# Kernel optimization log

Measured on AMD Instinct MI355X. Metric: run time of the kernel, lower is better.

Reference implementation:

```python
import jax, jax.numpy as jnp
import numpy as np

# Static problem sizes (see shape_source)
B, D, H, W = 2, 16, 64, 64          # batch, sparse_shape = grid_size[::-1]
NV = 20000                           # active voxels per batch sample
CIN = 16                             # input_channels
THRESH = 0.5                         # FOCAL_THRESHOLD (used for kernel-offset mask)
EPS = 1e-3                           # BatchNorm eps from norm_fn
K_FORE = int(NV * THRESH)            # topk split: top int(N*threshold) voxels are foreground
# kernel_offsets: [[i,j,k] for i,j,k in (-1..1)^3] minus [0,0,0], applied to [z,y,x]
OFFSETS = [(i, j, k) for i in range(-1, 2) for j in range(-1, 2) for k in range(-1, 2) if (i, j, k) != (0, 0, 0)]


def _conv(x, w):
    # dense 3x3x3 conv == SubMConv3d math at active sites (inactive cells hold zeros)
    return jax.lax.conv_general_dilated(x, w, (1, 1, 1), 'SAME',
                                        dimension_numbers=('NDHWC', 'DHWIO', 'NDHWC'))


def _bn(x, g, b, m, v):
    # eval-mode BatchNorm1d over voxel features
    return (x - m) * (g * jax.lax.rsqrt(v + EPS)) + b


def setup_inputs() -> dict:
    rng = np.random.default_rng(0)
    coords = []
    for b in range(B):  # unique voxel coords per sample (spconv requires unique indices)
        lin = rng.permutation(D * H * W)[:NV]
        z = lin // (H * W); r = lin % (H * W)
        coords.append(np.stack([np.full(NV, b), z, r // W, r % W], 1))
    voxel_coords = jnp.asarray(np.concatenate(coords, 0), jnp.int32)  # [B*NV, 4] = [b,z,y,x]
    ks = jax.random.split(jax.random.key(0), 24)

    def bn_p(i, c):
        return (1.0 + 0.1 * jax.random.normal(ks[i], (c,)),
                0.1 * jax.random.normal(ks[i + 1], (c,)),
                0.1 * jax.random.normal(ks[i + 2], (c,)),
                jax.random.uniform(ks[i + 3], (c,), minval=0.5, maxval=1.5))

    g1, b1, m1, v1 = bn_p(4, 32)
    g2, b2, m2, v2 = bn_p(8, 64)
    g3, b3, m3, v3 = bn_p(12, 128)
    return dict(
        voxel_features=jax.random.normal(ks[0], (B * NV, CIN), jnp.float32),
        voxel_coords=voxel_coords,
        w1=0.08 * jax.random.normal(ks[1], (3, 3, 3, CIN, 32), jnp.float32),
        w2=0.06 * jax.random.normal(ks[2], (3, 3, 3, 32, 64), jnp.float32),
        w_imp=0.05 * jax.random.normal(ks[3], (3, 3, 3, 64, 27), jnp.float32),
        w_focal=0.04 * jax.random.normal(ks[16], (3, 3, 3, 64, 128), jnp.float32),
        g1=g1, b1=b1, m1=m1, v1=v1,
        g2=g2, b2=b2, m2=m2, v2=v2,
        g3=g3, b3=b3, m3=m3, v3=v3)


def reference(voxel_features, w1, g1, b1, m1, v1, w2, g2, b2, m2, v2,
              w_imp, w_focal, g3, b3, m3, v3, voxel_coords):
    bi, z, y, x = (voxel_coords[:, i] for i in range(4))
    # scatter sparse voxels into dense grid; zeros at inactive cells
    dense = jnp.zeros((B, D, H, W, CIN), voxel_features.dtype).at[bi, z, y, x].set(voxel_features)
    active = jnp.zeros((B, D, H, W), bool).at[bi, z, y, x].set(True)
    am = active[..., None].astype(voxel_features.dtype)

    # conv_input: two SubMConv3d + BN + ReLU (re-mask so inactive cells stay zero)
    h = jax.nn.relu(_bn(_conv(dense, w1), g1, b1, m1, v1)) * am   # -> 32
    h = jax.nn.relu(_bn(_conv(h, w2), g2, b2, m2, v2)) * am       # -> 64

    # conv_imp -> 27 logits; last = voxel importance, first 26 = kernel-offset importances
    imp = _conv(h, w_imp)
    mask_voxel = jax.nn.sigmoid(imp[..., -1])
    mask_kernel = jax.nn.sigmoid(imp[..., :26])

    # split_voxels with topk=True: foreground = top int(NV*thr) voxels per batch by importance
    mv_flat = jnp.where(active, mask_voxel, -jnp.inf).reshape(B, -1)
    kth = jax.lax.top_k(mv_flat, K_FORE)[0][:, -1]
    fore = active & (mask_voxel >= kth[:, None, None, None])

    # dilate foreground by kernel offsets where offset importance >= threshold.
    # New voxels carry zero features; check_repeat (index_add dedup) then reduces to:
    # final features == original features, final actives == active OR dilated candidates.
    new_act = active
    for i, (oz, oy, ox) in enumerate(OFFSETS):
        src = fore & (mask_kernel[..., i] >= THRESH)
        p = jnp.pad(src, ((0, 0), (1, 1), (1, 1), (1, 1)))  # zero(False)-pad for shift
        sh = p[:, 1 - oz:1 - oz + D, 1 - oy:1 - oy + H, 1 - ox:1 - ox + W]
        # original bound check is strict (>0), so plane 0 of each axis is invalid
        sh = sh.at[:, 0].set(False).at[:, :, 0].set(False).at[:, :, :, 0].set(False)
        new_act = new_act | sh

    # conv_focal on merged sparse set (new voxels have zero features -> dense conv matches)
    out = jax.nn.relu(_bn(_conv(h, w_focal), g3, b3, m3, v3)) * new_act[..., None].astype(h.dtype)
    return out  # densified encoded_spconv_tensor features [B, D, H, W, 128]
```

## Files before the change

kernel.cpp:

```cpp
#include <hip/hip_runtime.h>
#include <stdint.h>

#define Dd 16
#define Hh 64
#define Ww 64
#define NACT 40000
#define NVb 20000
#define KFORE 10000
#define EPSf 0.001f

typedef __attribute__((ext_vector_type(8))) short short8;
typedef __attribute__((ext_vector_type(4))) float f32x4;
typedef __attribute__((ext_vector_type(4))) unsigned short us4;

static __device__ __forceinline__ uint32_t f2sort(float f) {
    uint32_t u = __float_as_uint(f);
    return (u & 0x80000000u) ? ~u : (u | 0x80000000u);
}

static __device__ __forceinline__ unsigned short f2b(float f) {
    uint32_t u = __float_as_uint(f);
    return (unsigned short)((u + 0x7FFFu + ((u >> 16) & 1u)) >> 16);
}

static __device__ __forceinline__ int xcd_swz(int orig, int nwg) {
    int xcd = orig & 7, idx = orig >> 3;
    int q = nwg >> 3, r = nwg & 7;
    int base = xcd < r ? xcd * (q + 1) : r * (q + 1) + (xcd - r) * q;
    return base + idx;
}

__global__ void __launch_bounds__(256) k_scatter(const float* __restrict__ feat,
                                                 const int* __restrict__ coords,
                                                 float* __restrict__ dense16,
                                                 uint8_t* __restrict__ active,
                                                 uint8_t* __restrict__ new_act) {
    int i = blockIdx.x * 256 + threadIdx.x;
    if (i >= NACT) return;
    int b = coords[i * 4 + 0], z = coords[i * 4 + 1], y = coords[i * 4 + 2], x = coords[i * 4 + 3];
    int pos = ((b * Dd + z) * Hh + y) * Ww + x;
    active[pos] = 1;
    new_act[pos] = 1;
    const float4* f4 = (const float4*)(feat + (size_t)i * 16);
    float4* d4 = (float4*)(dense16 + (size_t)pos * 16);
    d4[0] = f4[0]; d4[1] = f4[1]; d4[2] = f4[2]; d4[3] = f4[3];
}

__global__ void __launch_bounds__(256) k_cnt(const uint8_t* __restrict__ mask,
                                             int* __restrict__ bcnt) {
    __shared__ int s[256];
    const int i = blockIdx.x * 256 + threadIdx.x;
    s[threadIdx.x] = mask[i] ? 1 : 0;
    __syncthreads();
    for (int off = 128; off > 0; off >>= 1) {
        if (threadIdx.x < off) s[threadIdx.x] += s[threadIdx.x + off];
        __syncthreads();
    }
    if (threadIdx.x == 0) bcnt[blockIdx.x] = s[0];
}

__global__ void __launch_bounds__(512) k_scan(const int* __restrict__ bcnt,
                                              int* __restrict__ boff, int* __restrict__ count) {
    __shared__ int s[512];
    const int t = threadIdx.x;
    const int v0 = bcnt[t];
    s[t] = v0;
    __syncthreads();
    for (int off = 1; off < 512; off <<= 1) {
        int v = s[t];
        if (t >= off) v += s[t - off];
        __syncthreads();
        s[t] = v;
        __syncthreads();
    }
    boff[t] = s[t] - v0;
    if (t == 511) *count = s[511];
}

__global__ void __launch_bounds__(256) k_emit(const uint8_t* __restrict__ mask,
                                              const int* __restrict__ boff,
                                              int* __restrict__ list) {
    __shared__ int s[256];
    const int i = blockIdx.x * 256 + threadIdx.x;
    const int pred = mask[i] ? 1 : 0;
    s[threadIdx.x] = pred;
    __syncthreads();
    for (int off = 1; off < 256; off <<= 1) {
        int v = s[threadIdx.x];
        if (threadIdx.x >= off) v += s[threadIdx.x - off];
        __syncthreads();
        s[threadIdx.x] = v;
        __syncthreads();
    }
    if (pred) list[boff[blockIdx.x] + s[threadIdx.x] - 1] = i;
}

__global__ void __launch_bounds__(256) k_conv1p(const int* __restrict__ list,
        const float* __restrict__ dense16, const float* __restrict__ w1,
        float* __restrict__ pbuf) {
    const int gb = xcd_swz(blockIdx.x, 157 * 3);
    const int chunk = gb / 3, tp = gb % 3;
    const int i = chunk * 256 + threadIdx.x;
    if (i >= NACT) return;
    const int pos = list[i];
    const int z = (pos >> 12) & 15, y = (pos >> 6) & 63, x = pos & 63;
    float acc[32];
    #pragma unroll
    for (int c = 0; c < 32; ++c) acc[c] = 0.f;
    const int dz = tp - 1;
    if ((unsigned)(z + dz) < Dd) {
        for (int tt = 0; tt < 9; ++tt) {
            const int dy = tt / 3 - 1, dx = tt % 3 - 1;
            if (!((unsigned)(y + dy) < Hh && (unsigned)(x + dx) < Ww)) continue;
            const float* row = dense16 + (size_t)(pos + dz * 4096 + dy * 64 + dx) * 16;
            const float* wt = w1 + (tp * 9 + tt) * 512;
            #pragma unroll
            for (int k4 = 0; k4 < 4; ++k4) {
                float4 xv = *(const float4*)(row + k4 * 4);
                float xs[4] = {xv.x, xv.y, xv.z, xv.w};
                #pragma unroll
                for (int j = 0; j < 4; ++j)
                    #pragma unroll
                    for (int c = 0; c < 32; ++c)
                        acc[c] = fmaf(xs[j], wt[(k4 * 4 + j) * 32 + c], acc[c]);
            }
        }
    }
    #pragma unroll
    for (int c = 0; c < 32; ++c) pbuf[(size_t)(tp * 32 + c) * NACT + i] = acc[c];
}

__global__ void __launch_bounds__(256) k_conv1c(const int* __restrict__ list,
        const float* __restrict__ pbuf,
        const float* __restrict__ g, const float* __restrict__ bta,
        const float* __restrict__ mu, const float* __restrict__ va,
        float* __restrict__ h1) {
    const int i = blockIdx.x * 256 + threadIdx.x;
    if (i >= NACT) return;
    const int pos = list[i];
    float res[32];
    #pragma unroll
    for (int c = 0; c < 32; ++c) {
        float s = pbuf[(size_t)c * NACT + i]
                + pbuf[(size_t)(32 + c) * NACT + i]
                + pbuf[(size_t)(64 + c) * NACT + i];
        const float sc = g[c] * (1.0f / sqrtf(va[c] + EPSf));
        res[c] = fmaxf(0.f, fmaf(s - mu[c], sc, bta[c]));
    }
    #pragma unroll
    for (int c4 = 0; c4 < 8; ++c4)
        *(float4*)(h1 + (size_t)pos * 32 + c4 * 4) = *(float4*)&res[c4 * 4];
}

__global__ void __launch_bounds__(256) k_conv2p(const int* __restrict__ list,
        const float* __restrict__ h1, const float* __restrict__ w2,
        float* __restrict__ pbuf) {
    const int gb = xcd_swz(blockIdx.x, 157 * 3);
    const int chunk = gb / 3, tp = gb % 3;
    const int i = chunk * 256 + threadIdx.x;
    if (i >= NACT) return;
    const int pos = list[i];
    const int z = (pos >> 12) & 15, y = (pos >> 6) & 63, x = pos & 63;
    float acc[64];
    #pragma unroll
    for (int c = 0; c < 64; ++c) acc[c] = 0.f;
    const int dz = tp - 1;
    if ((unsigned)(z + dz) < Dd) {
        for (int tt = 0; tt < 9; ++tt) {
            const int dy = tt / 3 - 1, dx = tt % 3 - 1;
            if (!((unsigned)(y + dy) < Hh && (unsigned)(x + dx) < Ww)) continue;
            const float* row = h1 + (size_t)(pos + dz * 4096 + dy * 64 + dx) * 32;
            const float* wt = w2 + (tp * 9 + tt) * 2048;
            #pragma unroll
            for (int k4 = 0; k4 < 8; ++k4) {
                float4 xv = *(const float4*)(row + k4 * 4);
                float xs[4] = {xv.x, xv.y, xv.z, xv.w};
                #pragma unroll
                for (int j = 0; j < 4; ++j)
                    #pragma unroll
                    for (int c = 0; c < 64; ++c)
                        acc[c] = fmaf(xs[j], wt[(k4 * 4 + j) * 64 + c], acc[c]);
            }
        }
    }
    #pragma unroll
    for (int c = 0; c < 64; ++c) pbuf[(size_t)(tp * 64 + c) * NACT + i] = acc[c];
}

__global__ void __launch_bounds__(256) k_conv2c(const int* __restrict__ list,
        const float* __restrict__ pbuf,
        const float* __restrict__ g, const float* __restrict__ bta,
        const float* __restrict__ mu, const float* __restrict__ va,
        float* __restrict__ h2, unsigned short* __restrict__ h2b) {
    const int i = blockIdx.x * 256 + threadIdx.x;
    if (i >= NACT) return;
    const int pos = list[i];
    float res[64];
    #pragma unroll
    for (int c = 0; c < 64; ++c) {
        float s = pbuf[(size_t)c * NACT + i]
                + pbuf[(size_t)(64 + c) * NACT + i]
                + pbuf[(size_t)(128 + c) * NACT + i];
        const float sc = g[c] * (1.0f / sqrtf(va[c] + EPSf));
        res[c] = fmaxf(0.f, fmaf(s - mu[c], sc, bta[c]));
    }
    #pragma unroll
    for (int c4 = 0; c4 < 16; ++c4)
        *(float4*)(h2 + (size_t)pos * 64 + c4 * 4) = *(float4*)&res[c4 * 4];
    #pragma unroll
    for (int c4 = 0; c4 < 16; ++c4) {
        us4 o = { f2b(res[c4 * 4]), f2b(res[c4 * 4 + 1]), f2b(res[c4 * 4 + 2]), f2b(res[c4 * 4 + 3]) };
        *(us4*)(h2b + (size_t)pos * 64 + c4 * 4) = o;
    }
}

__global__ void __launch_bounds__(256) k_impp(const int* __restrict__ list,
        const float* __restrict__ h2, const float* __restrict__ wimp,
        float* __restrict__ pbuf) {
    const int gb = xcd_swz(blockIdx.x, 157 * 9);
    const int chunk = gb / 9, tp = gb % 9;
    const int i = chunk * 256 + threadIdx.x;
    if (i >= NACT) return;
    const int pos = list[i];
    const int z = (pos >> 12) & 15, y = (pos >> 6) & 63, x = pos & 63;
    float acc[27];
    #pragma unroll
    for (int c = 0; c < 27; ++c) acc[c] = 0.f;
    for (int tt = 0; tt < 3; ++tt) {
        const int t = tp * 3 + tt;
        const int dz = t / 9 - 1, dy = (t / 3) % 3 - 1, dx = t % 3 - 1;
        if (!((unsigned)(z + dz) < Dd && (unsigned)(y + dy) < Hh && (unsigned)(x + dx) < Ww)) continue;
        const float* row = h2 + (size_t)(pos + dz * 4096 + dy * 64 + dx) * 64;
        const float* wt = wimp + t * 1728;
        #pragma unroll
        for (int k4 = 0; k4 < 16; ++k4) {
            float4 xv = *(const float4*)(row + k4 * 4);
            float xs[4] = {xv.x, xv.y, xv.z, xv.w};
            #pragma unroll
            for (int j = 0; j < 4; ++j)
                #pragma unroll
                for (int c = 0; c < 27; ++c)
                    acc[c] = fmaf(xs[j], wt[(k4 * 4 + j) * 27 + c], acc[c]);
        }
    }
    #pragma unroll
    for (int c = 0; c < 27; ++c) pbuf[(size_t)(tp * 27 + c) * NACT + i] = acc[c];
}

__global__ void __launch_bounds__(256) k_impc(const float* __restrict__ pbuf,
        uint32_t* __restrict__ u_logits, uint32_t* __restrict__ kbits) {
    const int i = blockIdx.x * 256 + threadIdx.x;
    if (i >= NACT) return;
    uint32_t bits = 0;
    float logit = 0.f;
    #pragma unroll
    for (int c = 0; c < 27; ++c) {
        float s = 0.f;
        #pragma unroll
        for (int tp = 0; tp < 9; ++tp)
            s += pbuf[(size_t)(tp * 27 + c) * NACT + i];
        if (c < 26) bits |= (s >= 0.f ? 1u : 0u) << c;
        else logit = s;
    }
    kbits[i] = bits;
    u_logits[i] = f2sort(logit);
}

__global__ void __launch_bounds__(256) k_select(const uint32_t* __restrict__ u_all,
                                                uint32_t* __restrict__ kth_u) {
    const int b = blockIdx.x;
    const uint32_t* u = u_all + (size_t)b * NVb;
    __shared__ int hist[256];
    __shared__ int s_d, s_above;
    uint32_t prefix = 0;
    int K = KFORE;
    for (int p = 3; p >= 0; --p) {
        hist[threadIdx.x] = 0;
        __syncthreads();
        const int sh = p * 8;
        for (int i = threadIdx.x; i < NVb; i += 256) {
            uint32_t ui = u[i];
            bool cand;
            if (p == 3) cand = true;
            else cand = ((ui >> (sh + 8)) == prefix);
            if (cand) atomicAdd(&hist[(ui >> sh) & 255], 1);
        }
        __syncthreads();
        if (threadIdx.x == 0) {
            int cum = 0, d = 255;
            for (; d >= 0; --d) { cum += hist[d]; if (cum >= K) break; }
            s_d = d; s_above = cum - hist[d];
        }
        __syncthreads();
        prefix = (prefix << 8) | (uint32_t)s_d;
        K -= s_above;
        __syncthreads();
    }
    if (threadIdx.x == 0) kth_u[b] = prefix;
}

__global__ void __launch_bounds__(256) k_dilate(const int* __restrict__ list,
                                                const uint32_t* __restrict__ u_logits,
                                                const uint32_t* __restrict__ kbits,
                                                const uint32_t* __restrict__ kth_u,
                                                uint8_t* __restrict__ new_act) {
    int i = blockIdx.x * 256 + threadIdx.x;
    if (i >= NACT) return;
    int pos = list[i];
    int b = pos >> 16;
    if (u_logits[i] < kth_u[b]) return;
    int z = (pos >> 12) & 15, y = (pos >> 6) & 63, x = pos & 63;
    uint32_t bits = kbits[i];
    while (bits) {
        int ch = __ffs(bits) - 1;
        bits &= bits - 1;
        int l = ch + (ch >= 13 ? 1 : 0);
        int oz = l / 9 - 1, oy = (l / 3) % 3 - 1, ox = l % 3 - 1;
        int tz = z + oz, ty = y + oy, tx = x + ox;
        if (tz >= 1 && tz < Dd && ty >= 1 && ty < Hh && tx >= 1 && tx < Ww)
            new_act[((b * Dd + tz) * Hh + ty) * Ww + tx] = 1;
    }
}

__global__ void __launch_bounds__(256) k_wcvt(const float* __restrict__ wf,
                                              unsigned short* __restrict__ wfb) {
    int i = blockIdx.x * 256 + threadIdx.x;
    int t = i >> 13, r = i & 8191, n = r >> 6, k = r & 63;
    wfb[i] = f2b(wf[(t * 64 + k) * 128 + n]);
}

__global__ void __launch_bounds__(256, 4) k_focal(
        const int* __restrict__ list, const int* __restrict__ count,
        const unsigned short* __restrict__ h2b, const unsigned short* __restrict__ wfb,
        const float* __restrict__ g, const float* __restrict__ bta,
        const float* __restrict__ mu, const float* __restrict__ va,
        float* __restrict__ out, const unsigned short* __restrict__ zb) {
    __shared__ __align__(16) unsigned short As[2][64 * 64];
    __shared__ int s_pos[64];
    const int n = *count;
    const int i0 = xcd_swz(blockIdx.x, 2048) * 64;
    if (i0 >= n) return;
    const int tid = threadIdx.x;
    const int wv = tid >> 6, lane = tid & 63;
    if (tid < 64) { int idx = i0 + tid; s_pos[tid] = idx < n ? list[idx] : -1; }
    __syncthreads();
    const int v0 = tid >> 3, c8 = tid & 7, v1 = v0 + 32;
    const int p0 = s_pos[v0], p1 = s_pos[v1];
    const int z0 = (p0 >> 12) & 15, y0 = (p0 >> 6) & 63, x0 = p0 & 63;
    const int z1 = (p1 >> 12) & 15, y1 = (p1 >> 6) & 63, x1 = p1 & 63;
    const int wslot = (c8 ^ (v0 & 7)) << 3;
    const int wa0 = v0 * 64 + wslot, wa1 = v1 * 64 + wslot;
    const int hi = lane >> 4, lo = lane & 15;
    const int cb = wv * 32;

    f32x4 acc[4][2];
    #pragma unroll
    for (int mi = 0; mi < 4; ++mi)
        #pragma unroll
        for (int ni = 0; ni < 2; ++ni) acc[mi][ni] = (f32x4){0.f, 0.f, 0.f, 0.f};

    auto gather = [&](int t, short8& r0, short8& r1) {
        int dz = t / 9 - 1, dy = (t / 3) % 3 - 1, dx = t % 3 - 1;
        int off = dz * 4096 + dy * 64 + dx;
        bool ok0 = p0 >= 0 && (unsigned)(z0 + dz) < Dd && (unsigned)(y0 + dy) < Hh && (unsigned)(x0 + dx) < Ww;
        bool ok1 = p1 >= 0 && (unsigned)(z1 + dz) < Dd && (unsigned)(y1 + dy) < Hh && (unsigned)(x1 + dx) < Ww;
        r0 = *(const short8*)(ok0 ? h2b + (size_t)(p0 + off) * 64 + c8 * 8 : zb);
        r1 = *(const short8*)(ok1 ? h2b + (size_t)(p1 + off) * 64 + c8 * 8 : zb);
    };

    auto compute = [&](int t, int buf) {
        short8 bfr[2][2];
        #pragma unroll
        for (int ni = 0; ni < 2; ++ni)
            #pragma unroll
            for (int ks = 0; ks < 2; ++ks)
                bfr[ni][ks] = *(const short8*)(wfb + (size_t)t * 8192
                                + (size_t)(cb + ni * 16 + lo) * 64 + ks * 32 + hi * 8);
        #pragma unroll
        for (int ks = 0; ks < 2; ++ks) {
            const int rs = ((ks * 4 + hi) ^ (lo & 7)) << 3;
            short8 a[4];
            #pragma unroll
            for (int mi = 0; mi < 4; ++mi)
                a[mi] = *(const short8*)&As[buf][(mi * 16 + lo) * 64 + rs];
            #pragma unroll
            for (int mi = 0; mi < 4; ++mi)
                #pragma unroll
                for (int ni = 0; ni < 2; ++ni)
                    acc[mi][ni] = __builtin_amdgcn_mfma_f32_16x16x32_bf16(
                        a[mi], bfr[ni][ks], acc[mi][ni], 0, 0, 0);
        }
    };

    short8 rA0, rA1, rB0, rB1;
    gather(0, rA0, rA1);
    gather(1, rB0, rB1);
    *(short8*)&As[0][wa0] = rA0; *(short8*)&As[0][wa1] = rA1;
    *(short8*)&As[1][wa0] = rB0; *(short8*)&As[1][wa1] = rB1;
    gather(2, rA0, rA1);
    gather(3, rB0, rB1);
    __syncthreads();

    for (int t = 0; t < 26; t += 2) {
        compute(t, 0);
        __syncthreads();
        if (t + 2 <= 26) {
            *(short8*)&As[0][wa0] = rA0;
            *(short8*)&As[0][wa1] = rA1;
            if (t + 4 <= 26) gather(t + 4, rA0, rA1);
        }
        compute(t + 1, 1);
        __syncthreads();
        if (t + 3 <= 26) {
            *(short8*)&As[1][wa0] = rB0;
            *(short8*)&As[1][wa1] = rB1;
            if (t + 5 <= 26) gather(t + 5, rB0, rB1);
        }
        if (t + 2 > 26) break;
    }
    __syncthreads();
    compute(26, 0);

    #pragma unroll
    for (int ni = 0; ni < 2; ++ni) {
        const int ch = cb + ni * 16 + lo;
        const float s = g[ch] * (1.0f / sqrtf(va[ch] + EPSf));
        const float sh = bta[ch], mm = mu[ch];
        #pragma unroll
        for (int mi = 0; mi < 4; ++mi)
            #pragma unroll
            for (int j = 0; j < 4; ++j) {
                int vi = mi * 16 + hi * 4 + j;
                if (i0 + vi < n)
                    out[(size_t)s_pos[vi] * 128 + ch] = fmaxf(0.f, fmaf(acc[mi][ni][j] - mm, s, sh));
            }
    }
}

extern "C" void kernel_launch(void* const* d_in, const int* in_sizes, int n_in,
                              void* d_out, int out_size, void* d_ws, size_t ws_size,
                              hipStream_t stream) {
    (void)in_sizes; (void)n_in; (void)ws_size;
    const float* feat   = (const float*)d_in[0];
    const int*   coords = (const int*)d_in[1];
    const float* w1   = (const float*)d_in[2];
    const float* w2   = (const float*)d_in[3];
    const float* wimp = (const float*)d_in[4];
    const float* wf   = (const float*)d_in[5];
    const float* g1 = (const float*)d_in[6],  *b1 = (const float*)d_in[7];
    const float* m1 = (const float*)d_in[8],  *v1 = (const float*)d_in[9];
    const float* g2 = (const float*)d_in[10], *b2 = (const float*)d_in[11];
    const float* m2 = (const float*)d_in[12], *v2 = (const float*)d_in[13];
    const float* g3 = (const float*)d_in[14], *b3 = (const float*)d_in[15];
    const float* m3 = (const float*)d_in[16], *v3 = (const float*)d_in[17];

    char* ws = (char*)d_ws;
    float*    dense16  = (float*)(ws + 0);
    float*    h1       = (float*)(ws + 8388608);
    float*    h2       = (float*)(ws + 25165824);
    uint8_t*  active   = (uint8_t*)(ws + 58720256);
    uint8_t*  new_act  = (uint8_t*)(ws + 58851328);
    float*    zrow     = (float*)(ws + 58982400);
    int*      count    = (int*)(ws + 58982656);
    const size_t MEMSET_BYTES = 58982912;
    uint32_t* u_logits = (uint32_t*)(ws + 58982912);
    uint32_t* kbits    = (uint32_t*)(ws + 59142912);
    uint32_t* kth_u    = (uint32_t*)(ws + 59302912);
    int*      list     = (int*)(ws + 59303168);

    unsigned short* wfb = (unsigned short*)dense16;
    unsigned short* h2b = (unsigned short*)h1;
    float* pbuf = (float*)d_out;
    int* bcnt = (int*)kbits;
    int* boff = (int*)kbits + 512;

    hipMemsetAsync(d_ws, 0, MEMSET_BYTES, stream);

    k_scatter<<<157, 256, 0, stream>>>(feat, coords, dense16, active, new_act);
    k_cnt<<<512, 256, 0, stream>>>(active, bcnt);
    k_scan<<<1, 512, 0, stream>>>(bcnt, boff, count);
    k_emit<<<512, 256, 0, stream>>>(active, boff, list);
    k_conv1p<<<157 * 3, 256, 0, stream>>>(list, dense16, w1, pbuf);
    k_conv1c<<<157, 256, 0, stream>>>(list, pbuf, g1, b1, m1, v1, h1);
    k_wcvt<<<864, 256, 0, stream>>>(wf, wfb);
    k_conv2p<<<157 * 3, 256, 0, stream>>>(list, h1, w2, pbuf);
    hipMemsetAsync(h2b, 0, (size_t)131072 * 64 * 2, stream);
    k_conv2c<<<157, 256, 0, stream>>>(list, pbuf, g2, b2, m2, v2, h2, h2b);
    k_impp<<<157 * 9, 256, 0, stream>>>(list, h2, wimp, pbuf);
    k_impc<<<157, 256, 0, stream>>>(pbuf, u_logits, kbits);
    hipMemsetAsync(d_out, 0, (size_t)out_size * sizeof(float), stream);
    k_select<<<2, 256, 0, stream>>>(u_logits, kth_u);
    k_dilate<<<157, 256, 0, stream>>>(list, u_logits, kbits, kth_u, new_act);
    k_cnt<<<512, 256, 0, stream>>>(new_act, bcnt);
    k_scan<<<1, 512, 0, stream>>>(bcnt, boff, count);
    k_emit<<<512, 256, 0, stream>>>(new_act, boff, list);
    k_focal<<<2048, 256, 0, stream>>>(list, count, h2b, wfb, g3, b3, m3, v3,
                                      (float*)d_out, (const unsigned short*)zrow);
}
```

Measured before the change: 646.2 us.

## Stage gathered neighbor rows in shared memory and split output channels across threads

The conv2 and importance partial kernels now handle 64 voxels per block. Each tap's neighbor rows are gathered cooperatively into padded shared memory, and each thread computes a subset of output channels (16 for conv2, 7 for importance) instead of all of them. This cuts per-thread register pressure (64 and 27 accumulators before), coalesces the gathers and raises the block count, aiming for better occupancy and memory efficiency. The cost is extra barriers per tap and some wasted lanes in the importance kernel, where 27 channels do not divide evenly across 4 groups.

```diff
diff --git a/kernel.cpp b/kernel.cpp
--- a/kernel.cpp
+++ b/kernel.cpp
@@ -155,36 +155,51 @@
 __global__ void __launch_bounds__(256) k_conv2p(const int* __restrict__ list,
         const float* __restrict__ h1, const float* __restrict__ w2,
         float* __restrict__ pbuf) {
-    const int gb = xcd_swz(blockIdx.x, 157 * 3);
+    __shared__ float S[64 * 33];
+    __shared__ int s_pos[64];
+    const int gb = xcd_swz(blockIdx.x, 625 * 3);
     const int chunk = gb / 3, tp = gb % 3;
-    const int i = chunk * 256 + threadIdx.x;
-    if (i >= NACT) return;
-    const int pos = list[i];
-    const int z = (pos >> 12) & 15, y = (pos >> 6) & 63, x = pos & 63;
-    float acc[64];
-    #pragma unroll
-    for (int c = 0; c < 64; ++c) acc[c] = 0.f;
+    const int tid = threadIdx.x;
+    if (tid < 64) s_pos[tid] = list[chunk * 64 + tid];
+    __syncthreads();
+    const int v = tid & 63, og = tid >> 6;
+    const int cb = og * 16;
+    const int sr = tid >> 3, sc = tid & 7;
     const int dz = tp - 1;
-    if ((unsigned)(z + dz) < Dd) {
-        for (int tt = 0; tt < 9; ++tt) {
-            const int dy = tt / 3 - 1, dx = tt % 3 - 1;
-            if (!((unsigned)(y + dy) < Hh && (unsigned)(x + dx) < Ww)) continue;
-            const float* row = h1 + (size_t)(pos + dz * 4096 + dy * 64 + dx) * 32;
-            const float* wt = w2 + (tp * 9 + tt) * 2048;
-            #pragma unroll
-            for (int k4 = 0; k4 < 8; ++k4) {
-                float4 xv = *(const float4*)(row + k4 * 4);
-                float xs[4] = {xv.x, xv.y, xv.z, xv.w};
-                #pragma unroll
-                for (int j = 0; j < 4; ++j)
-                    #pragma unroll
-                    for (int c = 0; c < 64; ++c)
-                        acc[c] = fmaf(xs[j], wt[(k4 * 4 + j) * 64 + c], acc[c]);
-            }
-        }
-    }
-    #pragma unroll
-    for (int c = 0; c < 64; ++c) pbuf[(size_t)(tp * 64 + c) * NACT + i] = acc[c];
+    float acc[16];
+    #pragma unroll
+    for (int c = 0; c < 16; ++c) acc[c] = 0.f;
+
+    for (int tt = 0; tt < 9; ++tt) {
+        const int dy = tt / 3 - 1, dx = tt % 3 - 1;
+        const int off = dz * 4096 + dy * 64 + dx;
+        #pragma unroll
+        for (int p = 0; p < 2; ++p) {
+            const int r = p * 32 + sr;
+            const int pos = s_pos[r];
+            const int z = (pos >> 12) & 15, y = (pos >> 6) & 63, x = pos & 63;
+            bool ok = (unsigned)(z + dz) < Dd && (unsigned)(y + dy) < Hh && (unsigned)(x + dx) < Ww;
+            float4 val = ok ? *(const float4*)(h1 + (size_t)(pos + off) * 32 + sc * 4)
+                            : (float4){0.f, 0.f, 0.f, 0.f};
+            float* d = &S[r * 33 + sc * 4];
+            d[0] = val.x; d[1] = val.y; d[2] = val.z; d[3] = val.w;
+        }
+        __syncthreads();
+        const float* wt = w2 + (tp * 9 + tt) * 2048 + cb;
+        const float* myrow = &S[v * 33];
+        #pragma unroll 8
+        for (int k = 0; k < 32; ++k) {
+            const float xv = myrow[k];
+            #pragma unroll
+            for (int j = 0; j < 16; ++j)
+                acc[j] = fmaf(xv, wt[k * 64 + j], acc[j]);
+        }
+        __syncthreads();
+    }
+    const int i = chunk * 64 + v;
+    #pragma unroll
+    for (int j = 0; j < 16; ++j)
+        pbuf[(size_t)(tp * 64 + cb + j) * NACT + i] = acc[j];
 }
 
 __global__ void __launch_bounds__(256) k_conv2c(const int* __restrict__ list,
@@ -217,34 +232,55 @@
 __global__ void __launch_bounds__(256) k_impp(const int* __restrict__ list,
         const float* __restrict__ h2, const float* __restrict__ wimp,
         float* __restrict__ pbuf) {
-    const int gb = xcd_swz(blockIdx.x, 157 * 9);
+    __shared__ float S[64 * 65];
+    __shared__ int s_pos[64];
+    const int gb = xcd_swz(blockIdx.x, 625 * 9);
     const int chunk = gb / 9, tp = gb % 9;
-    const int i = chunk * 256 + threadIdx.x;
-    if (i >= NACT) return;
-    const int pos = list[i];
-    const int z = (pos >> 12) & 15, y = (pos >> 6) & 63, x = pos & 63;
-    float acc[27];
-    #pragma unroll
-    for (int c = 0; c < 27; ++c) acc[c] = 0.f;
+    const int tid = threadIdx.x;
+    if (tid < 64) s_pos[tid] = list[chunk * 64 + tid];
+    __syncthreads();
+    const int v = tid & 63, og = tid >> 6;
+    const int sr = tid >> 4, sc = tid & 15;
+    float acc[7];
+    #pragma unroll
+    for (int c = 0; c < 7; ++c) acc[c] = 0.f;
+
     for (int tt = 0; tt < 3; ++tt) {
         const int t = tp * 3 + tt;
         const int dz = t / 9 - 1, dy = (t / 3) % 3 - 1, dx = t % 3 - 1;
-        if (!((unsigned)(z + dz) < Dd && (unsigned)(y + dy) < Hh && (unsigned)(x + dx) < Ww)) continue;
-        const float* row = h2 + (size_t)(pos + dz * 4096 + dy * 64 + dx) * 64;
+        const int off = dz * 4096 + dy * 64 + dx;
+        #pragma unroll
+        for (int p = 0; p < 4; ++p) {
+            const int r = p * 16 + sr;
+            const int pos = s_pos[r];
+            const int z = (pos >> 12) & 15, y = (pos >> 6) & 63, x = pos & 63;
+            bool ok = (unsigned)(z + dz) < Dd && (unsigned)(y + dy) < Hh && (unsigned)(x + dx) < Ww;
+            float4 val = ok ? *(const float4*)(h2 + (size_t)(pos + off) * 64 + sc * 4)
+                            : (float4){0.f, 0.f, 0.f, 0.f};
+            float* d = &S[r * 65 + sc * 4];
+            d[0] = val.x; d[1] = val.y; d[2] = val.z; d[3] = val.w;
+        }
+        __syncthreads();
         const float* wt = wimp + t * 1728;
-        #pragma unroll
-        for (int k4 = 0; k4 < 16; ++k4) {
-            float4 xv = *(const float4*)(row + k4 * 4);
-            float xs[4] = {xv.x, xv.y, xv.z, xv.w};
-            #pragma unroll
-            for (int j = 0; j < 4; ++j)
-                #pragma unroll
-                for (int c = 0; c < 27; ++c)
-                    acc[c] = fmaf(xs[j], wt[(k4 * 4 + j) * 27 + c], acc[c]);
-        }
-    }
-    #pragma unroll
-    for (int c = 0; c < 27; ++c) pbuf[(size_t)(tp * 27 + c) * NACT + i] = acc[c];
+        const float* myrow = &S[v * 65];
+        #pragma unroll 8
+        for (int k = 0; k < 64; ++k) {
+            const float xv = myrow[k];
+            #pragma unroll
+            for (int j = 0; j < 7; ++j) {
+                const int och = og * 7 + j;
+                const int coch = och < 27 ? och : 26;
+                acc[j] = fmaf(xv, wt[k * 27 + coch], acc[j]);
+            }
+        }
+        __syncthreads();
+    }
+    const int i = chunk * 64 + v;
+    #pragma unroll
+    for (int j = 0; j < 7; ++j) {
+        const int och = og * 7 + j;
+        if (och < 27) pbuf[(size_t)(tp * 27 + och) * NACT + i] = acc[j];
+    }
 }
 
 __global__ void __launch_bounds__(256) k_impc(const float* __restrict__ pbuf,
@@ -483,10 +519,10 @@
     k_conv1p<<<157 * 3, 256, 0, stream>>>(list, dense16, w1, pbuf);
     k_conv1c<<<157, 256, 0, stream>>>(list, pbuf, g1, b1, m1, v1, h1);
     k_wcvt<<<864, 256, 0, stream>>>(wf, wfb);
-    k_conv2p<<<157 * 3, 256, 0, stream>>>(list, h1, w2, pbuf);
+    k_conv2p<<<625 * 3, 256, 0, stream>>>(list, h1, w2, pbuf);
     hipMemsetAsync(h2b, 0, (size_t)131072 * 64 * 2, stream);
     k_conv2c<<<157, 256, 0, stream>>>(list, pbuf, g2, b2, m2, v2, h2, h2b);
-    k_impp<<<157 * 9, 256, 0, stream>>>(list, h2, wimp, pbuf);
+    k_impp<<<625 * 9, 256, 0, stream>>>(list, h2, wimp, pbuf);
     k_impc<<<157, 256, 0, stream>>>(pbuf, u_logits, kbits);
     hipMemsetAsync(d_out, 0, (size_t)out_size * sizeof(float), stream);
     k_select<<<2, 256, 0, stream>>>(u_logits, kth_u);
```

Measured after the change: 965.4 us. 1.49x slower.
